# Kernel optimization log

Hardware: AMD Instinct MI355X
Metric: run time of the kernel (lower is better)

The kernel has to match this reference:

```python
import jax, jax.numpy as jnp
import numpy as np

N_HEAD = 16
N_KV_GROUP = 4
WINDOW = 256


def setup_inputs() -> dict:
    key = jax.random.key(0)
    ks = jax.random.split(key, 5)
    B, T, C = 2, 2048, 1024
    KV = C // N_HEAD * N_KV_GROUP  # 256
    s = 0.02
    return {
        "x": jax.random.normal(ks[0], (B, T, C), jnp.float32),
        "Wq": jax.random.normal(ks[1], (C, C), jnp.float32) * s,
        "bq": jnp.zeros((C,), jnp.float32),
        "Wk": jax.random.normal(ks[2], (C, KV), jnp.float32) * s,
        "bk": jnp.zeros((KV,), jnp.float32),
        "Wv": jax.random.normal(ks[3], (C, KV), jnp.float32) * s,
        "bv": jnp.zeros((KV,), jnp.float32),
        "Wo": jax.random.normal(ks[4], (C, C), jnp.float32) * s,
        "bo": jnp.zeros((C,), jnp.float32),
    }


def reference(x, Wq, bq, Wk, bk, Wv, bv, Wo, bo):
    B, T, C = x.shape
    hd = C // N_HEAD  # head dim = 64
    n_rep = N_HEAD // N_KV_GROUP

    q = x @ Wq + bq                      # [B,T,C]
    k = x @ Wk + bk                      # [B,T,KV]
    v = x @ Wv + bv

    q = q.reshape(B, T, N_HEAD, hd).transpose(0, 2, 1, 3)       # [B,H,T,d]
    k = k.reshape(B, T, N_KV_GROUP, hd).transpose(0, 2, 1, 3)   # [B,G,T,d]
    v = v.reshape(B, T, N_KV_GROUP, hd).transpose(0, 2, 1, 3)

    # GQA: repeat_interleave kv heads along head dim
    k_rep = jnp.repeat(k, n_rep, axis=1)                         # [B,H,T,d]
    v_rep = jnp.repeat(v, n_rep, axis=1)

    att = jnp.einsum("bhqd,bhkd->bhqk", q, k_rep) / jnp.sqrt(jnp.float32(hd))

    # causal + sliding window band mask: q position i attends to j in [i-WINDOW, i]
    i = jnp.arange(T)[:, None]
    j = jnp.arange(T)[None, :]
    band = (j <= i) & (j >= i - WINDOW)                           # [T,T]
    att = jnp.where(band[None, None], att, jnp.float32(-jnp.inf))

    att = jax.nn.softmax(att, axis=-1)
    y = jnp.einsum("bhqk,bhkd->bhqd", att, v_rep)                 # [B,H,T,d]
    y = y.transpose(0, 2, 1, 3).reshape(B, T, C)
    return y @ Wo + bo
```

## Files before the change

### kernel.cpp

```cpp
#include <hip/hip_runtime.h>
#include <hip/hip_bf16.h>

#define TT 2048
#define CC 1024
#define KVD 256
#define QKVD 1536

typedef __bf16 bf16x8 __attribute__((ext_vector_type(8)));
typedef float f32x4 __attribute__((ext_vector_type(4)));

__device__ __forceinline__ void gload_lds16(const __hip_bfloat16* g, __hip_bfloat16* l) {
  __builtin_amdgcn_global_load_lds(
      (const __attribute__((address_space(1))) unsigned int*)g,
      (__attribute__((address_space(3))) unsigned int*)l, 16, 0, 0);
}


__global__ __launch_bounds__(256) void k_prep(const float* __restrict__ x,
                                              const float* __restrict__ Wq,
                                              const float* __restrict__ Wk,
                                              const float* __restrict__ Wv,
                                              const float* __restrict__ Wo,
                                              const float* __restrict__ bq,
                                              const float* __restrict__ bk,
                                              const float* __restrict__ bv,
                                              __hip_bfloat16* __restrict__ xbf,
                                              __hip_bfloat16* __restrict__ wqkvT,
                                              __hip_bfloat16* __restrict__ woT,
                                              float* __restrict__ bqkv) {
  const int bxid = blockIdx.x;
  if (bxid < 4096) {
    size_t idx = ((size_t)bxid * 256 + threadIdx.x) * 4;
    float4 v = *(const float4*)(x + idx);
    xbf[idx + 0] = __float2bfloat16(v.x);
    xbf[idx + 1] = __float2bfloat16(v.y);
    xbf[idx + 2] = __float2bfloat16(v.z);
    xbf[idx + 3] = __float2bfloat16(v.w);
    return;
  }
  if (bxid == 4736) {
    for (int i = threadIdx.x; i < 1536; i += 256) {
      float v;
      if (i < 1024)      v = bq[i];
      else if (i < 1280) v = bk[i - 1024];
      else               v = bv[i - 1280];
      bqkv[i] = v;
    }
    return;
  }
  __shared__ float tile[64][65];
  const float* src;
  int ncols, k0, n0;
  __hip_bfloat16* dst;
  if (bxid < 4480) {
    const int idx = bxid - 4096;
    k0 = (idx & 15) * 64;
    n0 = (idx >> 4) * 64;
    dst = wqkvT;
    if (n0 < 1024)      { src = Wq; ncols = 1024; }
    else if (n0 < 1280) { src = Wk - 1024; ncols = 256; }
    else                { src = Wv - 1280; ncols = 256; }
  } else {
    const int idx = bxid - 4480;
    k0 = (idx & 15) * 64;
    n0 = (idx >> 4) * 64;
    dst = woT; src = Wo; ncols = 1024;
  }
  const int rw = threadIdx.x >> 6;
  const int cl = threadIdx.x & 63;
#pragma unroll
  for (int i = 0; i < 16; ++i) {
    const int kr = rw + i * 4;
    tile[kr][cl] = src[(size_t)(k0 + kr) * ncols + n0 + cl];
  }
  __syncthreads();
#pragma unroll
  for (int i = 0; i < 16; ++i) {
    const int nr = rw + i * 4;
    dst[(size_t)(n0 + nr) * 1024 + k0 + cl] = __float2bfloat16(tile[cl][nr]);
  }
}


template <bool OUT_BF16, bool SPLIT_V>
__global__ __launch_bounds__(256, 3) void k_gemm_bt(const __hip_bfloat16* __restrict__ A,
                                                    const __hip_bfloat16* __restrict__ BT,
                                                    const float* __restrict__ bias,
                                                    void* __restrict__ C,
                                                    __hip_bfloat16* __restrict__ vtg,
                                                    int M, int N, int K) {
  __shared__ __hip_bfloat16 As[2][64][64];
  __shared__ __hip_bfloat16 Bs[2][128][64];

  const int tid  = threadIdx.x;
  const int m0   = blockIdx.y * 64;
  const int n0   = blockIdx.x * 128;
  const int w    = tid >> 6;
  const int lane = tid & 63;
  const int quad = lane >> 4;
  const int l16  = lane & 15;
  const int wm   = (w >> 1) * 32;
  const int wn   = (w & 1) * 64;

  const int dl_r = lane >> 3;
  const int dl_c = (lane & 7) ^ dl_r;

  const __hip_bfloat16* gA = A + (size_t)(m0 + w * 16 + dl_r) * K + dl_c * 8;
  const __hip_bfloat16* gB = BT + (size_t)(n0 + w * 32 + dl_r) * K + dl_c * 8;

  f32x4 acc[2][4] = {};

  const int nk = K >> 6;

  {
    gload_lds16(gA,                  &As[0][w * 16][0]);
    gload_lds16(gA + (size_t)8 * K,  &As[0][w * 16 + 8][0]);
    gload_lds16(gB,                  &Bs[0][w * 32][0]);
    gload_lds16(gB + (size_t)8 * K,  &Bs[0][w * 32 + 8][0]);
    gload_lds16(gB + (size_t)16 * K, &Bs[0][w * 32 + 16][0]);
    gload_lds16(gB + (size_t)24 * K, &Bs[0][w * 32 + 24][0]);
  }

  int buf = 0;
  for (int kt = 0; kt < nk; ++kt) {
    __syncthreads();
    if (kt + 1 < nk) {
      const int k0 = (kt + 1) << 6;
      gload_lds16(gA + k0,                  &As[buf ^ 1][w * 16][0]);
      gload_lds16(gA + k0 + (size_t)8 * K,  &As[buf ^ 1][w * 16 + 8][0]);
      gload_lds16(gB + k0,                  &Bs[buf ^ 1][w * 32][0]);
      gload_lds16(gB + k0 + (size_t)8 * K,  &Bs[buf ^ 1][w * 32 + 8][0]);
      gload_lds16(gB + k0 + (size_t)16 * K, &Bs[buf ^ 1][w * 32 + 16][0]);
      gload_lds16(gB + k0 + (size_t)24 * K, &Bs[buf ^ 1][w * 32 + 24][0]);
    }

#pragma unroll
    for (int ks = 0; ks < 2; ++ks) {
      const int cb = (ks << 2) + quad;
      bf16x8 fa[2], fb[4];
#pragma unroll
      for (int i = 0; i < 2; ++i)
        fa[i] = *(const bf16x8*)&As[buf][wm + i * 16 + l16][(cb ^ (l16 & 7)) << 3];
#pragma unroll
      for (int j = 0; j < 4; ++j)
        fb[j] = *(const bf16x8*)&Bs[buf][wn + j * 16 + l16][(cb ^ (l16 & 7)) << 3];
#pragma unroll
      for (int i = 0; i < 2; ++i)
#pragma unroll
        for (int j = 0; j < 4; ++j)
          acc[i][j] = __builtin_amdgcn_mfma_f32_16x16x32_bf16(fa[i], fb[j], acc[i][j], 0, 0, 0);
    }
    buf ^= 1;
  }

#pragma unroll
  for (int j = 0; j < 4; ++j) {
    const int gn = n0 + wn + j * 16 + l16;
    const float bias_v = bias[gn];
    if (SPLIT_V && gn >= 1280) {
      const int dfull = gn - 1280;
      const int gg = dfull >> 6;
      const int dd = dfull & 63;
#pragma unroll
      for (int i = 0; i < 2; ++i) {
        const int gm = m0 + wm + i * 16 + quad * 4;
        const int bb = gm >> 11;
        const int tl = gm & 2047;
        __hip_bfloat16 tmp[4];
#pragma unroll
        for (int r = 0; r < 4; ++r) tmp[r] = __float2bfloat16(acc[i][j][r] + bias_v);
        *(uint2*)(vtg + ((size_t)((bb * 4 + gg) * 64 + dd)) * TT + tl) = *(const uint2*)tmp;
      }
    } else {
#pragma unroll
      for (int i = 0; i < 2; ++i) {
        const int gmb = m0 + wm + i * 16 + quad * 4;
#pragma unroll
        for (int r = 0; r < 4; ++r) {
          const float v = acc[i][j][r] + bias_v;
          const size_t idx = (size_t)(gmb + r) * N + gn;
          if (OUT_BF16) ((__hip_bfloat16*)C)[idx] = __float2bfloat16(v);
          else          ((float*)C)[idx] = v;
        }
      }
    }
  }
}


__global__ __launch_bounds__(256) void k_attn(const __hip_bfloat16* __restrict__ qkv,
                                              const __hip_bfloat16* __restrict__ vtg,
                                              __hip_bfloat16* __restrict__ y) {
  __shared__ __hip_bfloat16 Kb[2][64][64];
  __shared__ __hip_bfloat16 Vb[2][64][64];
  __shared__ __hip_bfloat16 Ps[4][16][72];

  const int t    = threadIdx.x;
  const int w    = t >> 6;
  const int lane = t & 63;
  const int quad = lane >> 4;
  const int l16  = lane & 15;
  const int bx   = blockIdx.x;
  const int h    = blockIdx.y;
  const int b    = blockIdx.z;
  const int g    = h >> 2;
  const int i0   = bx * 64;
  const int qrow      = i0 + w * 16 + l16;
  const int my_q_base = i0 + w * 16 + quad * 4;

  const int lrow = lane >> 3;
  const int cgl  = (lane & 7) ^ lrow;

  const __hip_bfloat16* kg =
      qkv + ((size_t)(b * TT + w * 16 + lrow)) * QKVD + 1024 + g * 64 + cgl * 8;
  const __hip_bfloat16* vg =
      vtg + ((size_t)((b * 4 + g) * 64 + w * 16 + lrow)) * TT + cgl * 8;

  bf16x8 fq[2];
  {
    const __hip_bfloat16* qp = qkv + ((size_t)(b * TT + qrow)) * QKVD + h * 64 + quad * 8;
    fq[0] = *(const bf16x8*)qp;
    fq[1] = *(const bf16x8*)(qp + 32);
  }

  float l_r[4] = {0.f, 0.f, 0.f, 0.f};
  f32x4 o_acc[4] = {};
  const float EC = 0.125f * 1.44269504f;

  const int c_lo = bx >= 4 ? bx - 4 : 0;

  {
    const size_t ko = (size_t)(c_lo * 64) * QKVD;
    gload_lds16(kg + ko,                    &Kb[0][w * 16][0]);
    gload_lds16(kg + ko + (size_t)8 * QKVD, &Kb[0][w * 16 + 8][0]);
    const int vo = c_lo * 64;
    gload_lds16(vg + vo,                  &Vb[0][w * 16][0]);
    gload_lds16(vg + vo + (size_t)8 * TT, &Vb[0][w * 16 + 8][0]);
  }

  int buf = 0;
  for (int c = c_lo; c <= bx; ++c) {
    __syncthreads();
    if (c < bx) {
      const size_t ko = (size_t)((c + 1) * 64) * QKVD;
      gload_lds16(kg + ko,                    &Kb[buf ^ 1][w * 16][0]);
      gload_lds16(kg + ko + (size_t)8 * QKVD, &Kb[buf ^ 1][w * 16 + 8][0]);
      const int vo = (c + 1) * 64;
      gload_lds16(vg + vo,                  &Vb[buf ^ 1][w * 16][0]);
      gload_lds16(vg + vo + (size_t)8 * TT, &Vb[buf ^ 1][w * 16 + 8][0]);
    }

    const int jc = c * 64;

    f32x4 sacc[4] = {};
#pragma unroll
    for (int ks = 0; ks < 2; ++ks) {
      const int sw = (((ks << 2) + quad) ^ (l16 & 7)) << 3;
#pragma unroll
      for (int nt = 0; nt < 4; ++nt) {
        const bf16x8 fk = *(const bf16x8*)&Kb[buf][nt * 16 + l16][sw];
        sacc[nt] = __builtin_amdgcn_mfma_f32_16x16x32_bf16(fq[ks], fk, sacc[nt], 0, 0, 0);
      }
    }

#pragma unroll
    for (int r = 0; r < 4; ++r) {
      const int gi = my_q_base + r;
      const int lo = gi - 256;
#pragma unroll
      for (int nt = 0; nt < 4; ++nt) {
        const int key = jc + nt * 16 + l16;
        const bool valid = (key <= gi) & (key >= lo);
        const float p = valid ? exp2f(sacc[nt][r] * EC) : 0.f;
        l_r[r] += p;
        Ps[w][quad * 4 + r][nt * 16 + l16] = __float2bfloat16(p);
      }
    }

    const bf16x8 fp0 = *(const bf16x8*)&Ps[w][l16][quad * 8];
    const bf16x8 fp1 = *(const bf16x8*)&Ps[w][l16][32 + quad * 8];

#pragma unroll
    for (int ks = 0; ks < 2; ++ks) {
      const int sw = (((ks << 2) + quad) ^ (l16 & 7)) << 3;
#pragma unroll
      for (int jt = 0; jt < 4; ++jt) {
        const bf16x8 fv = *(const bf16x8*)&Vb[buf][jt * 16 + l16][sw];
        o_acc[jt] = __builtin_amdgcn_mfma_f32_16x16x32_bf16(ks == 0 ? fp0 : fp1, fv,
                                                            o_acc[jt], 0, 0, 0);
      }
    }
    buf ^= 1;
  }

#pragma unroll
  for (int r = 0; r < 4; ++r) {
#pragma unroll
    for (int d = 1; d < 16; d <<= 1) l_r[r] += __shfl_xor(l_r[r], d);
    const float inv = 1.f / l_r[r];
    __hip_bfloat16* yp = y + ((size_t)(b * TT + my_q_base + r)) * CC + h * 64 + l16;
#pragma unroll
    for (int jt = 0; jt < 4; ++jt)
      yp[jt * 16] = __float2bfloat16(o_acc[jt][r] * inv);
  }
}


extern "C" void kernel_launch(void* const* d_in, const int* in_sizes, int n_in,
                              void* d_out, int out_size, void* d_ws, size_t ws_size,
                              hipStream_t stream) {
  const float* x  = (const float*)d_in[0];
  const float* Wq = (const float*)d_in[1];
  const float* bq = (const float*)d_in[2];
  const float* Wk = (const float*)d_in[3];
  const float* bk = (const float*)d_in[4];
  const float* Wv = (const float*)d_in[5];
  const float* bv = (const float*)d_in[6];
  const float* Wo = (const float*)d_in[7];
  const float* bo = (const float*)d_in[8];
  float* out = (float*)d_out;

  char* ws = (char*)d_ws;
  const size_t M = 2 * TT;
  __hip_bfloat16* xbf   = (__hip_bfloat16*)(ws);
  __hip_bfloat16* qkv   = (__hip_bfloat16*)(ws + 8388608);
  __hip_bfloat16* ybf   = (__hip_bfloat16*)(ws + 20971520);
  __hip_bfloat16* wqkvT = (__hip_bfloat16*)(ws + 29360128);
  __hip_bfloat16* woT   = (__hip_bfloat16*)(ws + 32505856);
  float*          bqkv  = (float*)(ws + 34603008);
  __hip_bfloat16* vtg   = (__hip_bfloat16*)(ws + 34609152);

  k_prep<<<4737, 256, 0, stream>>>(x, Wq, Wk, Wv, Wo, bq, bk, bv,
                                   xbf, wqkvT, woT, bqkv);

  k_gemm_bt<true, true><<<dim3(QKVD / 128, M / 64), 256, 0, stream>>>(
      xbf, wqkvT, bqkv, qkv, vtg, (int)M, QKVD, CC);

  k_attn<<<dim3(TT / 64, 16, 2), 256, 0, stream>>>(qkv, vtg, ybf);

  k_gemm_bt<false, false><<<dim3(CC / 128, M / 64), 256, 0, stream>>>(
      ybf, woT, bo, out, nullptr, (int)M, CC, CC);
}
```

Measured before the change: 146.6 us.

## Split GEMM into specialized kernels, enlarge QKV tile, single-buffer LDS, specialize attention masking

The templated GEMM becomes two kernels. The QKV projection uses 128x128 tiles with a 4x4 MFMA accumulator per wave, and the output projection uses single-buffered LDS with hardcoded K and an occupancy hint of 4. Both drop double buffering in favour of load-then-sync, which cuts LDS use but removes the overlap of global loads with compute. The attention kernel applies band-mask checks only on the diagonal and lowest key chunks, and full interior chunks skip masking entirely.

```diff
diff --git a/kernel.cpp b/kernel.cpp
--- a/kernel.cpp
+++ b/kernel.cpp
@@ -82,15 +82,97 @@
 }
 
 
-template <bool OUT_BF16, bool SPLIT_V>
-__global__ __launch_bounds__(256, 3) void k_gemm_bt(const __hip_bfloat16* __restrict__ A,
-                                                    const __hip_bfloat16* __restrict__ BT,
-                                                    const float* __restrict__ bias,
-                                                    void* __restrict__ C,
-                                                    __hip_bfloat16* __restrict__ vtg,
-                                                    int M, int N, int K) {
-  __shared__ __hip_bfloat16 As[2][64][64];
-  __shared__ __hip_bfloat16 Bs[2][128][64];
+__global__ __launch_bounds__(256, 3) void k_gemm1(const __hip_bfloat16* __restrict__ A,
+                                                  const __hip_bfloat16* __restrict__ BT,
+                                                  const float* __restrict__ bias,
+                                                  __hip_bfloat16* __restrict__ C,
+                                                  __hip_bfloat16* __restrict__ vtg) {
+  __shared__ __hip_bfloat16 As[128][64];
+  __shared__ __hip_bfloat16 Bs[128][64];
+
+  const int tid  = threadIdx.x;
+  const int m0   = blockIdx.y * 128;
+  const int n0   = blockIdx.x * 128;
+  const int w    = tid >> 6;
+  const int lane = tid & 63;
+  const int quad = lane >> 4;
+  const int l16  = lane & 15;
+  const int wm   = (w >> 1) * 64;
+  const int wn   = (w & 1) * 64;
+
+  const int dl_r = lane >> 3;
+  const int dl_c = (lane & 7) ^ dl_r;
+
+  const __hip_bfloat16* gA = A + (size_t)(m0 + w * 32 + dl_r) * 1024 + dl_c * 8;
+  const __hip_bfloat16* gB = BT + (size_t)(n0 + w * 32 + dl_r) * 1024 + dl_c * 8;
+
+  f32x4 acc[4][4] = {};
+
+  for (int kt = 0; kt < 16; ++kt) {
+    const int k0 = kt << 6;
+#pragma unroll
+    for (int rr = 0; rr < 4; ++rr) {
+      gload_lds16(gA + k0 + (size_t)(rr * 8) * 1024, &As[w * 32 + rr * 8][0]);
+      gload_lds16(gB + k0 + (size_t)(rr * 8) * 1024, &Bs[w * 32 + rr * 8][0]);
+    }
+    __syncthreads();
+
+#pragma unroll
+    for (int ks = 0; ks < 2; ++ks) {
+      const int cb = (ks << 2) + quad;
+      bf16x8 fa[4], fb[4];
+#pragma unroll
+      for (int i = 0; i < 4; ++i)
+        fa[i] = *(const bf16x8*)&As[wm + i * 16 + l16][(cb ^ (l16 & 7)) << 3];
+#pragma unroll
+      for (int j = 0; j < 4; ++j)
+        fb[j] = *(const bf16x8*)&Bs[wn + j * 16 + l16][(cb ^ (l16 & 7)) << 3];
+#pragma unroll
+      for (int i = 0; i < 4; ++i)
+#pragma unroll
+        for (int j = 0; j < 4; ++j)
+          acc[i][j] = __builtin_amdgcn_mfma_f32_16x16x32_bf16(fa[i], fb[j], acc[i][j], 0, 0, 0);
+    }
+    __syncthreads();
+  }
+
+#pragma unroll
+  for (int j = 0; j < 4; ++j) {
+    const int gn = n0 + wn + j * 16 + l16;
+    const float bias_v = bias[gn];
+    if (gn >= 1280) {
+      const int dfull = gn - 1280;
+      const int gg = dfull >> 6;
+      const int dd = dfull & 63;
+#pragma unroll
+      for (int i = 0; i < 4; ++i) {
+        const int gm = m0 + wm + i * 16 + quad * 4;
+        const int bb = gm >> 11;
+        const int tl = gm & 2047;
+        __hip_bfloat16 tmp[4];
+#pragma unroll
+        for (int r = 0; r < 4; ++r) tmp[r] = __float2bfloat16(acc[i][j][r] + bias_v);
+        *(uint2*)(vtg + ((size_t)((bb * 4 + gg) * 64 + dd)) * TT + tl) = *(const uint2*)tmp;
+      }
+    } else {
+#pragma unroll
+      for (int i = 0; i < 4; ++i) {
+        const int gmb = m0 + wm + i * 16 + quad * 4;
+#pragma unroll
+        for (int r = 0; r < 4; ++r)
+          C[(size_t)(gmb + r) * QKVD + gn] = __float2bfloat16(acc[i][j][r] + bias_v);
+      }
+    }
+  }
+}
+
+
+__global__ __launch_bounds__(256, 4) void k_gemm2(const __hip_bfloat16* __restrict__ A,
+                                                  const __hip_bfloat16* __restrict__ BT,
+                                                  const float* __restrict__ bias,
+                                                  float* __restrict__ C) {
+  __shared__ __hip_bfloat16 As[64][64];
+  __shared__ __hip_bfloat16 Bs[128][64];
 
   const int tid  = threadIdx.x;
   const int m0   = blockIdx.y * 64;
@@ -105,34 +187,20 @@
   const int dl_r = lane >> 3;
   const int dl_c = (lane & 7) ^ dl_r;
 
-  const __hip_bfloat16* gA = A + (size_t)(m0 + w * 16 + dl_r) * K + dl_c * 8;
-  const __hip_bfloat16* gB = BT + (size_t)(n0 + w * 32 + dl_r) * K + dl_c * 8;
+  const __hip_bfloat16* gA = A + (size_t)(m0 + w * 16 + dl_r) * 1024 + dl_c * 8;
+  const __hip_bfloat16* gB = BT + (size_t)(n0 + w * 32 + dl_r) * 1024 + dl_c * 8;
 
   f32x4 acc[2][4] = {};
 
-  const int nk = K >> 6;
-
-  {
-    gload_lds16(gA,                  &As[0][w * 16][0]);
-    gload_lds16(gA + (size_t)8 * K,  &As[0][w * 16 + 8][0]);
-    gload_lds16(gB,                  &Bs[0][w * 32][0]);
-    gload_lds16(gB + (size_t)8 * K,  &Bs[0][w * 32 + 8][0]);
-    gload_lds16(gB + (size_t)16 * K, &Bs[0][w * 32 + 16][0]);
-    gload_lds16(gB + (size_t)24 * K, &Bs[0][w * 32 + 24][0]);
-  }
-
-  int buf = 0;
-  for (int kt = 0; kt < nk; ++kt) {
+  for (int kt = 0; kt < 16; ++kt) {
+    const int k0 = kt << 6;
+    gload_lds16(gA + k0,                     &As[w * 16][0]);
+    gload_lds16(gA + k0 + (size_t)8 * 1024,  &As[w * 16 + 8][0]);
+    gload_lds16(gB + k0,                     &Bs[w * 32][0]);
+    gload_lds16(gB + k0 + (size_t)8 * 1024,  &Bs[w * 32 + 8][0]);
+    gload_lds16(gB + k0 + (size_t)16 * 1024, &Bs[w * 32 + 16][0]);
+    gload_lds16(gB + k0 + (size_t)24 * 1024, &Bs[w * 32 + 24][0]);
     __syncthreads();
-    if (kt + 1 < nk) {
-      const int k0 = (kt + 1) << 6;
-      gload_lds16(gA + k0,                  &As[buf ^ 1][w * 16][0]);
-      gload_lds16(gA + k0 + (size_t)8 * K,  &As[buf ^ 1][w * 16 + 8][0]);
-      gload_lds16(gB + k0,                  &Bs[buf ^ 1][w * 32][0]);
-      gload_lds16(gB + k0 + (size_t)8 * K,  &Bs[buf ^ 1][w * 32 + 8][0]);
-      gload_lds16(gB + k0 + (size_t)16 * K, &Bs[buf ^ 1][w * 32 + 16][0]);
-      gload_lds16(gB + k0 + (size_t)24 * K, &Bs[buf ^ 1][w * 32 + 24][0]);
-    }
 
 #pragma unroll
     for (int ks = 0; ks < 2; ++ks) {
@@ -140,49 +208,29 @@
       bf16x8 fa[2], fb[4];
 #pragma unroll
       for (int i = 0; i < 2; ++i)
-        fa[i] = *(const bf16x8*)&As[buf][wm + i * 16 + l16][(cb ^ (l16 & 7)) << 3];
+        fa[i] = *(const bf16x8*)&As[wm + i * 16 + l16][(cb ^ (l16 & 7)) << 3];
 #pragma unroll
       for (int j = 0; j < 4; ++j)
-        fb[j] = *(const bf16x8*)&Bs[buf][wn + j * 16 + l16][(cb ^ (l16 & 7)) << 3];
+        fb[j] = *(const bf16x8*)&Bs[wn + j * 16 + l16][(cb ^ (l16 & 7)) << 3];
 #pragma unroll
       for (int i = 0; i < 2; ++i)
 #pragma unroll
         for (int j = 0; j < 4; ++j)
           acc[i][j] = __builtin_amdgcn_mfma_f32_16x16x32_bf16(fa[i], fb[j], acc[i][j], 0, 0, 0);
     }
-    buf ^= 1;
+    __syncthreads();
   }
 
 #pragma unroll
   for (int j = 0; j < 4; ++j) {
     const int gn = n0 + wn + j * 16 + l16;
     const float bias_v = bias[gn];
-    if (SPLIT_V && gn >= 1280) {
-      const int dfull = gn - 1280;
-      const int gg = dfull >> 6;
-      const int dd = dfull & 63;
-#pragma unroll
-      for (int i = 0; i < 2; ++i) {
-        const int gm = m0 + wm + i * 16 + quad * 4;
-        const int bb = gm >> 11;
-        const int tl = gm & 2047;
-        __hip_bfloat16 tmp[4];
-#pragma unroll
-        for (int r = 0; r < 4; ++r) tmp[r] = __float2bfloat16(acc[i][j][r] + bias_v);
-        *(uint2*)(vtg + ((size_t)((bb * 4 + gg) * 64 + dd)) * TT + tl) = *(const uint2*)tmp;
-      }
-    } else {
-#pragma unroll
-      for (int i = 0; i < 2; ++i) {
-        const int gmb = m0 + wm + i * 16 + quad * 4;
-#pragma unroll
-        for (int r = 0; r < 4; ++r) {
-          const float v = acc[i][j][r] + bias_v;
-          const size_t idx = (size_t)(gmb + r) * N + gn;
-          if (OUT_BF16) ((__hip_bfloat16*)C)[idx] = __float2bfloat16(v);
-          else          ((float*)C)[idx] = v;
-        }
-      }
+#pragma unroll
+    for (int i = 0; i < 2; ++i) {
+      const int gmb = m0 + wm + i * 16 + quad * 4;
+#pragma unroll
+      for (int r = 0; r < 4; ++r)
+        C[(size_t)(gmb + r) * CC + gn] = acc[i][j][r] + bias_v;
     }
   }
 }
@@ -263,18 +311,39 @@
       }
     }
 
-#pragma unroll
-    for (int r = 0; r < 4; ++r) {
-      const int gi = my_q_base + r;
-      const int lo = gi - 256;
-#pragma unroll
-      for (int nt = 0; nt < 4; ++nt) {
-        const int key = jc + nt * 16 + l16;
-        const bool valid = (key <= gi) & (key >= lo);
-        const float p = valid ? exp2f(sacc[nt][r] * EC) : 0.f;
-        l_r[r] += p;
-        Ps[w][quad * 4 + r][nt * 16 + l16] = __float2bfloat16(p);
-      }
+    if (c == bx) {
+#pragma unroll
+      for (int r = 0; r < 4; ++r) {
+        const int gi = my_q_base + r;
+#pragma unroll
+        for (int nt = 0; nt < 4; ++nt) {
+          const int key = jc + nt * 16 + l16;
+          const float p = (key <= gi) ? exp2f(sacc[nt][r] * EC) : 0.f;
+          l_r[r] += p;
+          Ps[w][quad * 4 + r][nt * 16 + l16] = __float2bfloat16(p);
+        }
+      }
+    } else if (bx >= 4 && c == c_lo) {
+#pragma unroll
+      for (int r = 0; r < 4; ++r) {
+        const int glo = my_q_base + r - 256;
+#pragma unroll
+        for (int nt = 0; nt < 4; ++nt) {
+          const int key = jc + nt * 16 + l16;
+          const float p = (key >= glo) ? exp2f(sacc[nt][r] * EC) : 0.f;
+          l_r[r] += p;
+          Ps[w][quad * 4 + r][nt * 16 + l16] = __float2bfloat16(p);
+        }
+      }
+    } else {
+#pragma unroll
+      for (int r = 0; r < 4; ++r)
+#pragma unroll
+        for (int nt = 0; nt < 4; ++nt) {
+          const float p = exp2f(sacc[nt][r] * EC);
+          l_r[r] += p;
+          Ps[w][quad * 4 + r][nt * 16 + l16] = __float2bfloat16(p);
+        }
     }
 
     const bf16x8 fp0 = *(const bf16x8*)&Ps[w][l16][quad * 8];
@@ -333,11 +402,9 @@
   k_prep<<<4737, 256, 0, stream>>>(x, Wq, Wk, Wv, Wo, bq, bk, bv,
                                    xbf, wqkvT, woT, bqkv);
 
-  k_gemm_bt<true, true><<<dim3(QKVD / 128, M / 64), 256, 0, stream>>>(
-      xbf, wqkvT, bqkv, qkv, vtg, (int)M, QKVD, CC);
+  k_gemm1<<<dim3(QKVD / 128, M / 128), 256, 0, stream>>>(xbf, wqkvT, bqkv, qkv, vtg);
 
   k_attn<<<dim3(TT / 64, 16, 2), 256, 0, stream>>>(qkv, vtg, ybf);
 
-  k_gemm_bt<false, false><<<dim3(CC / 128, M / 64), 256, 0, stream>>>(
-      ybf, woT, bo, out, nullptr, (int)M, CC, CC);
-}
+  k_gemm2<<<dim3(CC / 128, M / 64), 256, 0, stream>>>(ybf, woT, bo, out);
+}
```

Measured after the change: 145.1 us. Within noise of the previous version (-1.0%).
